# Kernel optimization log

Measured on AMD Instinct MI355X. Metric: run time of the kernel, lower is better.

The kernel has to match this reference:

```python
import jax, jax.numpy as jnp
import numpy as np

Lc, Lq = 20, 50
CTX, CTXM = 2048, 512
NEG = -1e30


def setup_inputs() -> dict:
    key = jax.random.key(0)
    ks = jax.random.split(key, 8)
    B = 2048
    Vid_enc = jax.random.normal(ks[0], (B, Lc, CTX), dtype=jnp.float32)
    Ques_enc = jax.random.normal(ks[1], (B, CTXM, Lq), dtype=jnp.float32)
    V_mask = jnp.ones((B, Lc), dtype=jnp.float32)
    Q_mask = jnp.ones((B, Lq), dtype=jnp.float32)
    # weight-normed Linear(2048 -> 512): v [out,in], g [out], b [out]
    trans_v = jax.random.normal(ks[2], (CTXM, CTX), dtype=jnp.float32) * 0.02
    trans_g = jnp.linalg.norm(trans_v, axis=1)  # matches torch weight_norm init
    trans_b = jnp.zeros((CTXM,), dtype=jnp.float32)
    w4V = jax.random.normal(ks[3], (CTXM, 1), dtype=jnp.float32) * 0.05
    w4Q = jax.random.normal(ks[4], (CTXM, 1), dtype=jnp.float32) * 0.05
    w4mlu = jax.random.normal(ks[5], (1, 1, CTXM), dtype=jnp.float32) * 0.05
    bias = jnp.zeros((1,), dtype=jnp.float32)
    return {
        "Vid_enc": Vid_enc, "Ques_enc": Ques_enc,
        "V_mask": V_mask, "Q_mask": Q_mask,
        "trans_v": trans_v, "trans_g": trans_g, "trans_b": trans_b,
        "w4V": w4V, "w4Q": w4Q, "w4mlu": w4mlu, "bias": bias,
    }


def reference(Vid_enc, Ques_enc, V_mask, Q_mask,
              trans_v, trans_g, trans_b, w4V, w4Q, w4mlu, bias):
    # weight-normed linear projection: W = g * v / ||v||_row
    W = trans_g[:, None] * trans_v / jnp.linalg.norm(trans_v, axis=1, keepdims=True)
    V = jnp.einsum('blc,mc->blm', Vid_enc, W) + trans_b          # [B,Lc,512]
    Q = jnp.swapaxes(Ques_enc, 1, 2)                             # [B,Lq,512]
    # trilinear similarity (dropout p inactive at inference)
    s0 = V @ w4V                                                 # [B,Lc,1]
    s1 = jnp.swapaxes(Q @ w4Q, 1, 2)                             # [B,1,Lq]
    s2 = jnp.einsum('bld,bqd->blq', V * w4mlu, Q)                # [B,Lc,Lq]
    S = s0 + s1 + s2 + bias                                      # [B,Lc,Lq]
    Vm = V_mask[:, :, None]                                      # [B,Lc,1]
    Qm = Q_mask[:, None, :]                                      # [B,1,Lq]
    S1 = jax.nn.softmax(S * Qm + (1.0 - Qm) * NEG, axis=2)
    S2 = jax.nn.softmax(S * Vm + (1.0 - Vm) * NEG, axis=1)
    A = jnp.einsum('blq,bqd->bld', S1, Q)                        # [B,Lc,512]
    Bt = jnp.einsum('blq,bmq->blm', S1, S2)                      # [B,Lc,Lc]
    Bv = jnp.einsum('blm,bmd->bld', Bt, V)                       # [B,Lc,512]
    out = jnp.concatenate([V, A, V * A, V * Bv], axis=2)         # [B,Lc,2048]
    return jnp.swapaxes(out, 1, 2)                               # [B,2048,Lc]
```

## Files before the change

kernel.cpp:

```cpp
#include <hip/hip_runtime.h>
#include <math.h>

#define B_    2048
#define LC    20
#define LQ    50
#define CTX   2048
#define CTXM  512
#define NEGV  -1e30f

typedef __fp16 half8 __attribute__((ext_vector_type(8)));
typedef __fp16 f16x2 __attribute__((ext_vector_type(2)));
typedef float f32x4  __attribute__((ext_vector_type(4)));
typedef unsigned int uint;

__device__ __forceinline__ half8 cvt8v(float4 a, float4 b) {
    union { f16x2 h[4]; half8 v; } r;
    r.h[0] = __builtin_amdgcn_cvt_pkrtz(a.x, a.y);
    r.h[1] = __builtin_amdgcn_cvt_pkrtz(a.z, a.w);
    r.h[2] = __builtin_amdgcn_cvt_pkrtz(b.x, b.y);
    r.h[3] = __builtin_amdgcn_cvt_pkrtz(b.z, b.w);
    return r.v;
}
__device__ __forceinline__ half8 cvt8(const float* x) {
    union { f16x2 h[4]; half8 v; } r;
    r.h[0] = __builtin_amdgcn_cvt_pkrtz(x[0], x[1]);
    r.h[1] = __builtin_amdgcn_cvt_pkrtz(x[2], x[3]);
    r.h[2] = __builtin_amdgcn_cvt_pkrtz(x[4], x[5]);
    r.h[3] = __builtin_amdgcn_cvt_pkrtz(x[6], x[7]);
    return r.v;
}

#define GLOAD_LDS16(g, l)                                                        \
    __builtin_amdgcn_global_load_lds(                                            \
        (const __attribute__((address_space(1))) unsigned int*)(g),              \
        (__attribute__((address_space(3))) unsigned int*)(l), 16, 0, 0)

__global__ __launch_bounds__(256)
void scale_kernel(const float* __restrict__ trans_v,
                  const float* __restrict__ trans_g,
                  float* __restrict__ scale) {
    int m = blockIdx.x;
    int t = threadIdx.x;
    const float* row = trans_v + (size_t)m * CTX;
    float ss = 0.f;
    for (int i = t; i < CTX; i += 256) { float v = row[i]; ss += v * v; }
    __shared__ float red[256];
    red[t] = ss;
    __syncthreads();
    for (int s = 128; s > 0; s >>= 1) {
        if (t < s) red[t] += red[t + s];
        __syncthreads();
    }
    if (t == 0) scale[m] = trans_g[m] / sqrtf(red[0]);
}

__global__ __launch_bounds__(256)
void bpack_kernel(const float* __restrict__ Wt,
                  const float* __restrict__ scale,
                  char* __restrict__ Bp) {
    int u = blockIdx.x * 256 + threadIdx.x;
    size_t o = (size_t)u * 16;
    int nslab  = (int)(o >> 21);
    int rem    = (int)(o & 2097151);
    int kchunk = rem >> 15;
    int rem2   = rem & 32767;
    int r      = rem2 >> 7;
    int cphys  = rem2 & 127;
    int clog   = cphys ^ ((r & 7) << 4);
    int isLo   = clog >> 6;
    int k0     = kchunk * 32 + ((clog & 63) >> 1);
    int n      = nslab * 256 + r;
    float s = scale[n];
    const float* wr = Wt + (size_t)n * CTX + k0;
    union { __fp16 h[8]; uint4 u4; } out;
#pragma unroll
    for (int e = 0; e < 8; e++) {
        float w = wr[e] * s;
        __fp16 hi = (__fp16)w;
        out.h[e] = isLo ? (__fp16)(w - (float)hi) : hi;
    }
    *(uint4*)&Bp[o] = out.u4;
}

__global__ __launch_bounds__(512, 4)
void gemm_kernel(const float* __restrict__ A,
                 const char*  __restrict__ Bp,
                 const float* __restrict__ trans_b,
                 float* __restrict__ V)
{
    __shared__ char lds[81920] __attribute__((aligned(16)));

    int t = threadIdx.x;
    int orig = blockIdx.x;
    int wg = (orig & 7) * 80 + (orig >> 3);
    int nslab = wg & 1;
    int m0 = (wg >> 1) * 128;
    int n0 = nslab << 8;

    int wid = t >> 6, lane = t & 63;
    int l15 = lane & 15;
    int q16 = (lane >> 4) << 4;
    int ksl = lane >> 4;
    int rq  = (lane >> 4) << 2;
    int wm = (wid >> 2) << 6;
    int wn = (wid & 3) << 6;

    int r_a = t >> 2;
    int sl  = t & 3;
    int a_dst = 65536 + sl * 2048 + r_a * 16;
    const float* arow = A + (size_t)(m0 + r_a) * CTX + sl * 8;

    const char* bslab = Bp + (size_t)nslab * (64 * 32768);

    f32x4 acc[4][4];
#pragma unroll
    for (int i = 0; i < 4; i++)
#pragma unroll
        for (int j = 0; j < 4; j++) acc[i][j] = (f32x4){0.f, 0.f, 0.f, 0.f};

    {
        const char* src = bslab + t * 16;
#pragma unroll
        for (int i = 0; i < 4; i++)
            GLOAD_LDS16(src + i * 8192, lds + i * 8192 + t * 16);
    }
    float4 ra0 = *(const float4*)arow;
    float4 ra1 = *(const float4*)(arow + 4);

    int cur = 0;
    for (int it = 0; it < 64; ++it) {
        *(half8*)&lds[a_dst + cur * 8192] = cvt8v(ra0, ra1);
        __syncthreads();

        if (it + 1 < 64) {
            const char* src = bslab + (size_t)(it + 1) * 32768 + t * 16;
            char* dst = lds + (cur ^ 1) * 32768 + t * 16;
#pragma unroll
            for (int i = 0; i < 4; i++)
                GLOAD_LDS16(src + i * 8192, dst + i * 8192);
            ra0 = *(const float4*)(arow + (it + 1) * 32);
            ra1 = *(const float4*)(arow + (it + 1) * 32 + 4);
        }

        const char* Bb = lds + cur * 32768;
        const char* Ab = lds + 65536 + cur * 8192;
        half8 af[4];
#pragma unroll
        for (int mt = 0; mt < 4; mt++)
            af[mt] = *(const half8*)&Ab[ksl * 2048 + (wm + mt * 16 + l15) * 16];
#pragma unroll
        for (int nt = 0; nt < 4; nt++) {
            int r = wn + nt * 16 + l15;
            half8 bh = *(const half8*)&Bb[r * 128 + (q16 ^ ((r & 7) << 4))];
#pragma unroll
            for (int mt = 0; mt < 4; mt++)
                acc[mt][nt] = __builtin_amdgcn_mfma_f32_16x16x32_f16(af[mt], bh, acc[mt][nt], 0, 0, 0);
        }
#pragma unroll
        for (int nt = 0; nt < 4; nt++) {
            int r = wn + nt * 16 + l15;
            half8 bl = *(const half8*)&Bb[r * 128 + ((64 + q16) ^ ((r & 7) << 4))];
#pragma unroll
            for (int mt = 0; mt < 4; mt++)
                acc[mt][nt] = __builtin_amdgcn_mfma_f32_16x16x32_f16(af[mt], bl, acc[mt][nt], 0, 0, 0);
        }
        cur ^= 1;
    }

#pragma unroll
    for (int nt = 0; nt < 4; nt++) {
        int col = n0 + wn + nt * 16 + l15;
        float tb = trans_b[col];
#pragma unroll
        for (int mt = 0; mt < 4; mt++) {
            int m = m0 + wm + mt * 16 + rq;
#pragma unroll
            for (int rg = 0; rg < 4; rg++)
                V[(size_t)(m + rg) * CTXM + col] = acc[mt][nt][rg] + tb;
        }
    }
}

__global__ __launch_bounds__(512, 2)
void attn_kernel(const float* __restrict__ Ques,
                 const float* __restrict__ V_mask,
                 const float* __restrict__ Q_mask,
                 const float* __restrict__ w4V,
                 const float* __restrict__ w4Q,
                 const float* __restrict__ w4mlu,
                 const float* __restrict__ bias,
                 const float* __restrict__ V,
                 float* __restrict__ out)
{
    __shared__ __fp16 Qs[512 * 56 + 8];
    __shared__ float Ssh[LC][LQ];
    __shared__ float S1f[LC][LQ];
    __shared__ float S2f[LC][LQ];
    __shared__ __fp16 S1h[LC][72];
    __shared__ __fp16 S1l[LC][72];
    __shared__ __fp16 Bth[LC][40];
    __shared__ __fp16 Btl[LC][40];
    __shared__ float s1p[8][LQ];
    __shared__ float s0sh[LC];
    __shared__ float s1qsh[LQ];
    __shared__ float qmsh[LQ];
    __shared__ float vmsh[LC];

    int b = blockIdx.x;
    int t = threadIdx.x;
    int wid = t >> 6, lane = t & 63;
    int l15 = lane & 15;
    int kq  = (lane >> 4) << 3;
    int rq  = (lane >> 4) << 2;
    const float* Qb = Ques + (size_t)b * (CTXM * LQ);
    const float* Vb = V + (size_t)b * (LC * CTXM);

    if (t < LQ) qmsh[t] = Q_mask[(size_t)b * LQ + t];
    else if (t >= 64 && t < 64 + LC) vmsh[t - 64] = V_mask[(size_t)b * LC + (t - 64)];
    if (t < 8) Qs[512 * 56 + t] = (__fp16)0;

#pragma unroll
    for (int i = 0; i < 7; i++) {
        int task = t + 512 * i;
        int d  = task / 7;
        int sc = task - d * 7;
        const float* qr = Qb + (size_t)d * LQ + sc * 8;
        float xs[8];
        if (sc < 6) {
            float2 p0 = *(const float2*)&qr[0];
            float2 p1 = *(const float2*)&qr[2];
            float2 p2 = *(const float2*)&qr[4];
            float2 p3 = *(const float2*)&qr[6];
            xs[0] = p0.x; xs[1] = p0.y; xs[2] = p1.x; xs[3] = p1.y;
            xs[4] = p2.x; xs[5] = p2.y; xs[6] = p3.x; xs[7] = p3.y;
        } else {
            float2 p0 = *(const float2*)&qr[0];
            xs[0] = p0.x; xs[1] = p0.y;
            xs[2] = 0.f; xs[3] = 0.f; xs[4] = 0.f; xs[5] = 0.f;
            xs[6] = 0.f; xs[7] = 0.f;
        }
        *(half8*)&Qs[d * 56 + sc * 8] = cvt8(xs);
    }

    for (int l = wid; l < LC; l += 8) {
        float a = 0.f;
        const float* vr = Vb + (size_t)l * CTXM;
#pragma unroll
        for (int i = 0; i < CTXM / 64; i++)
            a = fmaf(vr[lane + 64 * i], w4V[lane + 64 * i], a);
#pragma unroll
        for (int o = 32; o > 0; o >>= 1) a += __shfl_xor(a, o);
        if (lane == 0) s0sh[l] = a;
    }
    __syncthreads();

    {
        int q = (lane < LQ) ? lane : (LQ - 1);
        float a = 0.f;
#pragma unroll
        for (int i = 0; i < 64; i++) {
            int d = (wid << 6) + i;
            a = fmaf((float)Qs[d * 56 + q], w4Q[d], a);
        }
        if (lane < LQ) s1p[wid][lane] = a;
    }

    int mt = wid >> 2, nt = wid & 3;
    f32x4 accS = {0.f, 0.f, 0.f, 0.f};
    {
        int lA = mt * 16 + l15; if (lA > LC - 1) lA = LC - 1;
        int qB = nt * 16 + l15; if (qB > LQ - 1) qB = LQ - 1;
        const float* vrow = Vb + (size_t)lA * CTXM;
        for (int kt = 0; kt < 16; kt++) {
            int d0 = kt * 32 + kq;
            float xa[8];
            float4 va = *(const float4*)&vrow[d0];
            float4 vc = *(const float4*)&vrow[d0 + 4];
            float4 wa = *(const float4*)&w4mlu[d0];
            float4 wc = *(const float4*)&w4mlu[d0 + 4];
            xa[0] = va.x * wa.x; xa[1] = va.y * wa.y; xa[2] = va.z * wa.z; xa[3] = va.w * wa.w;
            xa[4] = vc.x * wc.x; xa[5] = vc.y * wc.y; xa[6] = vc.z * wc.z; xa[7] = vc.w * wc.w;
            half8 vf = cvt8(xa);
            union { __fp16 h[8]; half8 v; } qq;
#pragma unroll
            for (int e = 0; e < 8; e++) qq.h[e] = Qs[(d0 + e) * 56 + qB];
            accS = __builtin_amdgcn_mfma_f32_16x16x32_f16(vf, qq.v, accS, 0, 0, 0);
        }
    }
    __syncthreads();

    if (t < LQ) {
        float s = 0.f;
#pragma unroll
        for (int w = 0; w < 8; w++) s += s1p[w][t];
        s1qsh[t] = s;
    }
    __syncthreads();

    {
        float bb = bias[0];
        int q = nt * 16 + l15;
#pragma unroll
        for (int r = 0; r < 4; r++) {
            int l = mt * 16 + rq + r;
            if (l < LC && q < LQ)
                Ssh[l][q] = accS[r] + s0sh[l] + s1qsh[q] + bb;
        }
    }
    __syncthreads();

    for (int l = wid; l < LC; l += 8) {
        float x;
        if (lane < LQ) {
            float qm = qmsh[lane];
            x = Ssh[l][lane] * qm + (1.f - qm) * NEGV;
        } else x = -INFINITY;
        float mx = x;
#pragma unroll
        for (int o = 32; o > 0; o >>= 1) mx = fmaxf(mx, __shfl_xor(mx, o));
        float e = (lane < LQ) ? expf(x - mx) : 0.f;
        float sum = e;
#pragma unroll
        for (int o = 32; o > 0; o >>= 1) sum += __shfl_xor(sum, o);
        float p = e / sum;
        if (lane < LQ) S1f[l][lane] = p;
        __fp16 hs = (__fp16)p;
        __fp16 ls = (__fp16)(p - (float)hs);
        S1h[l][lane] = (lane < LQ) ? hs : (__fp16)0;
        S1l[l][lane] = (lane < LQ) ? ls : (__fp16)0;
    }

    for (int ci = 0; ci < 7; ci++) {
        int c = wid * 7 + ci;
        if (c < LQ) {
            float x;
            if (lane < LC) {
                float vm = vmsh[lane];
                x = Ssh[lane][c] * vm + (1.f - vm) * NEGV;
            } else x = -INFINITY;
            float mx = x;
#pragma unroll
            for (int o = 32; o > 0; o >>= 1) mx = fmaxf(mx, __shfl_xor(mx, o));
            float e = (lane < LC) ? expf(x - mx) : 0.f;
            float sum = e;
#pragma unroll
            for (int o = 32; o > 0; o >>= 1) sum += __shfl_xor(sum, o);
            if (lane < LC) S2f[lane][c] = e / sum;
        }
    }
    __syncthreads();

    if (t < LC * LC) {
        int l = t % LC, m = t / LC;
        float s = 0.f;
#pragma unroll
        for (int j = 0; j < LQ; j++) s = fmaf(S1f[l][j], S2f[m][j], s);
        __fp16 hs = (__fp16)s;
        Bth[l][m] = hs;
        Btl[l][m] = (__fp16)(s - (float)hs);
    }
    if (t < 240) {
        int l = t % LC, m = LC + t / LC;
        Bth[l][m] = (__fp16)0; Btl[l][m] = (__fp16)0;
    }
    __syncthreads();

    float* outb = out + (size_t)b * (4 * CTXM * LC);
#pragma unroll 1
    for (int i = 0; i < 4; i++) {
        int dt = wid + 8 * i;
        int d0 = dt * 16;
        int dq = d0 + l15;
        half8 qf0 = *(const half8*)&Qs[dq * 56 + kq];
        half8 qf1 = *(const half8*)&Qs[dq * 56 + 32 + kq];
        float xv[8];
#pragma unroll
        for (int e = 0; e < 8; e++) {
            int m = kq + e;
            int mc = (m < LC) ? m : 0;
            float vv = Vb[(size_t)mc * CTXM + d0 + l15];
            xv[e] = (m < LC) ? vv : 0.f;
        }
        half8 vt = cvt8(xv);

        f32x4 accA[2] = {{0.f,0.f,0.f,0.f},{0.f,0.f,0.f,0.f}};
        f32x4 accB[2] = {{0.f,0.f,0.f,0.f},{0.f,0.f,0.f,0.f}};
#pragma unroll
        for (int n2 = 0; n2 < 2; n2++) {
            int lS = n2 * 16 + l15; if (lS > LC - 1) lS = LC - 1;
            half8 s1h0 = *(const half8*)&S1h[lS][kq];
            half8 s1l0 = *(const half8*)&S1l[lS][kq];
            half8 s1h1 = *(const half8*)&S1h[lS][32 + kq];
            half8 s1l1 = *(const half8*)&S1l[lS][32 + kq];
            accA[n2] = __builtin_amdgcn_mfma_f32_16x16x32_f16(qf0, s1h0, accA[n2], 0, 0, 0);
            accA[n2] = __builtin_amdgcn_mfma_f32_16x16x32_f16(qf0, s1l0, accA[n2], 0, 0, 0);
            accA[n2] = __builtin_amdgcn_mfma_f32_16x16x32_f16(qf1, s1h1, accA[n2], 0, 0, 0);
            accA[n2] = __builtin_amdgcn_mfma_f32_16x16x32_f16(qf1, s1l1, accA[n2], 0, 0, 0);
            half8 bh = *(const half8*)&Bth[lS][kq];
            half8 bl = *(const half8*)&Btl[lS][kq];
            accB[n2] = __builtin_amdgcn_mfma_f32_16x16x32_f16(vt, bh, accB[n2], 0, 0, 0);
            accB[n2] = __builtin_amdgcn_mfma_f32_16x16x32_f16(vt, bl, accB[n2], 0, 0, 0);
        }

#pragma unroll
        for (int n2 = 0; n2 < 2; n2++) {
            int l = n2 * 16 + l15;
            if (l < LC) {
#pragma unroll
                for (int r = 0; r < 4; r++) {
                    int d = d0 + rq + r;
                    float vv = Vb[(size_t)l * CTXM + d];
                    float a  = accA[n2][r];
                    float bv = accB[n2][r];
                    size_t base = (size_t)d * LC + l;
                    outb[base]                 = vv;
                    outb[base + CTXM * LC]     = a;
                    outb[base + 2 * CTXM * LC] = vv * a;
                    outb[base + 3 * CTXM * LC] = vv * bv;
                }
            }
        }
    }
}

extern "C" void kernel_launch(void* const* d_in, const int* in_sizes, int n_in,
                              void* d_out, int out_size, void* d_ws, size_t ws_size,
                              hipStream_t stream) {
    const float* Vid   = (const float*)d_in[0];
    const float* Ques  = (const float*)d_in[1];
    const float* Vmask = (const float*)d_in[2];
    const float* Qmask = (const float*)d_in[3];
    const float* tv    = (const float*)d_in[4];
    const float* tg    = (const float*)d_in[5];
    const float* tb    = (const float*)d_in[6];
    const float* w4V   = (const float*)d_in[7];
    const float* w4Q   = (const float*)d_in[8];
    const float* w4mlu = (const float*)d_in[9];
    const float* bias  = (const float*)d_in[10];
    float* out = (float*)d_out;

    float* scale = (float*)d_ws;
    float* V     = scale + 512;
    char*  Bp    = (char*)(V + (size_t)40960 * 512);

    scale_kernel<<<512, 256, 0, stream>>>(tv, tg, scale);
    bpack_kernel<<<1024, 256, 0, stream>>>(tv, scale, Bp);
    gemm_kernel<<<640, 512, 0, stream>>>(Vid, Bp, tb, V);
    attn_kernel<<<B_, 512, 0, stream>>>(Ques, Vmask, Qmask, w4V, w4Q, w4mlu, bias, V, out);
}
```

Before: 428.3 us.

## Halve GEMM block threads, give each wave a full 128-row M tile

The GEMM block drops from 8 waves to 4. Each wave now covers all 128 M rows and 64 N columns, so it holds 32 accumulator tiles instead of 16. The A tile in LDS moves from a k-slice-major layout to a row-pair layout with an XOR swizzle, which changes both the staging stores and the fragment reads. The goal is to reuse each B fragment across more MFMAs and cut LDS traffic per FLOP, at the cost of higher register pressure, fewer waves to hide latency, and more load work per thread.

```diff
diff --git a/kernel.cpp b/kernel.cpp
--- a/kernel.cpp
+++ b/kernel.cpp
@@ -82,7 +82,7 @@
     *(uint4*)&Bp[o] = out.u4;
 }
 
-__global__ __launch_bounds__(512, 4)
+__global__ __launch_bounds__(256, 2)
 void gemm_kernel(const float* __restrict__ A,
                  const char*  __restrict__ Bp,
                  const float* __restrict__ trans_b,
@@ -102,58 +102,71 @@
     int q16 = (lane >> 4) << 4;
     int ksl = lane >> 4;
     int rq  = (lane >> 4) << 2;
-    int wm = (wid >> 2) << 6;
-    int wn = (wid & 3) << 6;
-
-    int r_a = t >> 2;
-    int sl  = t & 3;
-    int a_dst = 65536 + sl * 2048 + r_a * 16;
-    const float* arow = A + (size_t)(m0 + r_a) * CTX + sl * 8;
+    int wn  = wid << 6;
+
+    int r_a = t >> 1;
+    int h_a = t & 1;
+    int rp_a = r_a >> 1;
+    int sw_a = (rp_a & 7) << 4;
+    int c0_a = (r_a & 1) * 64 + h_a * 32;
+    int a_d0 = 65536 + rp_a * 128 + ((c0_a) ^ sw_a);
+    int a_d1 = 65536 + rp_a * 128 + ((c0_a + 16) ^ sw_a);
+    const float* arow = A + (size_t)(m0 + r_a) * CTX + h_a * 16;
 
     const char* bslab = Bp + (size_t)nslab * (64 * 32768);
 
-    f32x4 acc[4][4];
-#pragma unroll
-    for (int i = 0; i < 4; i++)
+    f32x4 acc[8][4];
+#pragma unroll
+    for (int i = 0; i < 8; i++)
 #pragma unroll
         for (int j = 0; j < 4; j++) acc[i][j] = (f32x4){0.f, 0.f, 0.f, 0.f};
 
     {
         const char* src = bslab + t * 16;
 #pragma unroll
-        for (int i = 0; i < 4; i++)
-            GLOAD_LDS16(src + i * 8192, lds + i * 8192 + t * 16);
+        for (int i = 0; i < 8; i++)
+            GLOAD_LDS16(src + i * 4096, lds + i * 4096 + t * 16);
     }
     float4 ra0 = *(const float4*)arow;
     float4 ra1 = *(const float4*)(arow + 4);
+    float4 ra2 = *(const float4*)(arow + 8);
+    float4 ra3 = *(const float4*)(arow + 12);
 
     int cur = 0;
     for (int it = 0; it < 64; ++it) {
-        *(half8*)&lds[a_dst + cur * 8192] = cvt8v(ra0, ra1);
+        *(half8*)&lds[a_d0 + cur * 8192] = cvt8v(ra0, ra1);
+        *(half8*)&lds[a_d1 + cur * 8192] = cvt8v(ra2, ra3);
         __syncthreads();
 
         if (it + 1 < 64) {
             const char* src = bslab + (size_t)(it + 1) * 32768 + t * 16;
             char* dst = lds + (cur ^ 1) * 32768 + t * 16;
 #pragma unroll
-            for (int i = 0; i < 4; i++)
-                GLOAD_LDS16(src + i * 8192, dst + i * 8192);
-            ra0 = *(const float4*)(arow + (it + 1) * 32);
-            ra1 = *(const float4*)(arow + (it + 1) * 32 + 4);
+            for (int i = 0; i < 8; i++)
+                GLOAD_LDS16(src + i * 4096, dst + i * 4096);
+            int ko = (it + 1) * 32;
+            ra0 = *(const float4*)(arow + ko);
+            ra1 = *(const float4*)(arow + ko + 4);
+            ra2 = *(const float4*)(arow + ko + 8);
+            ra3 = *(const float4*)(arow + ko + 12);
         }
 
         const char* Bb = lds + cur * 32768;
         const char* Ab = lds + 65536 + cur * 8192;
-        half8 af[4];
-#pragma unroll
-        for (int mt = 0; mt < 4; mt++)
-            af[mt] = *(const half8*)&Ab[ksl * 2048 + (wm + mt * 16 + l15) * 16];
+        half8 af[8];
+#pragma unroll
+        for (int mt = 0; mt < 8; mt++) {
+            int r  = mt * 16 + l15;
+            int rp = r >> 1;
+            int c  = (r & 1) * 64 + ksl * 16;
+            af[mt] = *(const half8*)&Ab[rp * 128 + (c ^ ((rp & 7) << 4))];
+        }
 #pragma unroll
         for (int nt = 0; nt < 4; nt++) {
             int r = wn + nt * 16 + l15;
             half8 bh = *(const half8*)&Bb[r * 128 + (q16 ^ ((r & 7) << 4))];
 #pragma unroll
-            for (int mt = 0; mt < 4; mt++)
+            for (int mt = 0; mt < 8; mt++)
                 acc[mt][nt] = __builtin_amdgcn_mfma_f32_16x16x32_f16(af[mt], bh, acc[mt][nt], 0, 0, 0);
         }
 #pragma unroll
@@ -161,7 +174,7 @@
             int r = wn + nt * 16 + l15;
             half8 bl = *(const half8*)&Bb[r * 128 + ((64 + q16) ^ ((r & 7) << 4))];
 #pragma unroll
-            for (int mt = 0; mt < 4; mt++)
+            for (int mt = 0; mt < 8; mt++)
                 acc[mt][nt] = __builtin_amdgcn_mfma_f32_16x16x32_f16(af[mt], bl, acc[mt][nt], 0, 0, 0);
         }
         cur ^= 1;
@@ -172,8 +185,8 @@
         int col = n0 + wn + nt * 16 + l15;
         float tb = trans_b[col];
 #pragma unroll
-        for (int mt = 0; mt < 4; mt++) {
-            int m = m0 + wm + mt * 16 + rq;
+        for (int mt = 0; mt < 8; mt++) {
+            int m = m0 + mt * 16 + rq;
 #pragma unroll
             for (int rg = 0; rg < 4; rg++)
                 V[(size_t)(m + rg) * CTXM + col] = acc[mt][nt][rg] + tb;
@@ -445,6 +458,6 @@
 
     scale_kernel<<<512, 256, 0, stream>>>(tv, tg, scale);
     bpack_kernel<<<1024, 256, 0, stream>>>(tv, scale, Bp);
-    gemm_kernel<<<640, 512, 0, stream>>>(Vid, Bp, tb, V);
+    gemm_kernel<<<640, 256, 0, stream>>>(Vid, Bp, tb, V);
     attn_kernel<<<B_, 512, 0, stream>>>(Ques, Vmask, Qmask, w4V, w4Q, w4mlu, bias, V, out);
 }
```

Result: slower. 445.3 us (+4.0%).
